# Optimization experiments

Measured on AMD Instinct MI355X. Metric: run time of the kernel, lower is better.

Reference implementation:

```python
import jax, jax.numpy as jnp
import numpy as np

TOPK = 4  # constructor default topk=4


def setup_inputs() -> dict:
    key = jax.random.key(0)
    k_x, k_a, k_b, k_w, k_bias = jax.random.split(key, 5)
    b, s, h, j, a, r = 4, 2048, 2048, 2048, 64, 16
    x = jax.random.normal(k_x, (b, s, h), dtype=jnp.float32)
    A = jax.random.normal(k_a, (a, r, h), dtype=jnp.float32) * 0.02   # adapter down-proj bank
    B = jax.random.normal(k_b, (a, j, r), dtype=jnp.float32) * 0.02   # adapter up-proj bank
    W = jax.random.normal(k_w, (j, h), dtype=jnp.float32) * 0.02      # base Linear weight
    bias = jax.random.normal(k_bias, (j,), dtype=jnp.float32) * 0.02  # base Linear bias
    return {"x": x, "A": A, "B": B, "W": W, "bias": bias}


def reference(x, A, B, W, bias):
    # vecs: per-adapter low-rank projections of each token. [b,s,a,r]
    vecs = jnp.einsum('arh,bsh->bsar', A, x)
    # routing score = L2 norm over rank dim. [b,s,a]
    arrows = jnp.linalg.norm(vecs, axis=-1)
    # top-k adapters per token -> uniform 1/topk routing weights (scatter of a constant,
    # so no gradient flows through the routing weights, matching torch semantics).
    _, idx = jax.lax.top_k(arrows, TOPK)                     # [b,s,topk]
    routes = jax.nn.one_hot(idx, arrows.shape[-1], dtype=x.dtype).sum(-2) / TOPK  # [b,s,a]
    # weighted combine of selected adapter vecs. [b,s,r]
    v = jnp.einsum('bsa,bsar->bsr', routes, vecs)
    # delta = (routes-weighted B) applied to v; contract over a then r without
    # materializing the [b,s,j,r] intermediate. [b,s,j]
    delta = jnp.einsum('bsa,ajr,bsr->bsj', routes, B, v)
    base = jnp.einsum('bsh,jh->bsj', x, W) + bias
    return base + delta
```

## Files before the change

kernel.cpp:

```cpp
#include <hip/hip_runtime.h>
#include <hip/hip_bf16.h>
#include <stdint.h>

#define TOKENS 8192
#define H 2048
#define JDIM 2048
#define NADAPT 64
#define RANK 16
#define KG 1024
#define KTOT 3072
#define NT2 48
#define NT1 64

typedef __bf16 v8bf __attribute__((ext_vector_type(8)));
typedef float v4f __attribute__((ext_vector_type(4)));
typedef unsigned short us8 __attribute__((ext_vector_type(8)));
typedef unsigned short us4 __attribute__((ext_vector_type(4)));

__device__ __forceinline__ unsigned short f2bf(float f) {
  union { __bf16 b; unsigned short u; } c; c.b = (__bf16)f; return c.u;
}
__device__ __forceinline__ float bf2f(unsigned short u) {
  union { unsigned int u; float f; } c; c.u = ((unsigned int)u) << 16; return c.f;
}

__device__ __forceinline__ us8 pack8(float4 a, float4 b) {
  us8 r;
  r[0]=f2bf(a.x); r[1]=f2bf(a.y); r[2]=f2bf(a.z); r[3]=f2bf(a.w);
  r[4]=f2bf(b.x); r[5]=f2bf(b.y); r[6]=f2bf(b.z); r[7]=f2bf(b.w);
  return r;
}

__device__ __forceinline__ void split8(float4 a, float4 b, us8& h, us8& l) {
  float v[8] = {a.x, a.y, a.z, a.w, b.x, b.y, b.z, b.w};
  #pragma unroll
  for (int i = 0; i < 8; ++i) {
    h[i] = f2bf(v[i]);
    l[i] = f2bf(v[i] - bf2f(h[i]));
  }
}

__global__ void cast_x_split_kernel(const float* __restrict__ x,
                                    unsigned short* __restrict__ XG,
                                    unsigned short* __restrict__ XLO) {
  int idx = blockIdx.x * 256 + threadIdx.x;
  int row = idx >> 8;
  int cg  = idx & 255;
  const float4* s = (const float4*)(x + ((size_t)row << 11) + ((size_t)cg << 3));
  float4 a = s[0], b = s[1];
  us8 h, l;
  split8(a, b, h, l);
  *(us8*)(XG  + (size_t)row * KTOT + ((size_t)cg << 3)) = h;
  *(us8*)(XLO + (size_t)row * H    + ((size_t)cg << 3)) = l;
}

__global__ void cast_a_split_kernel(const float* __restrict__ A,
                                    unsigned short* __restrict__ Ahi,
                                    unsigned short* __restrict__ Alo) {
  int idx = blockIdx.x * 256 + threadIdx.x;
  int row = idx >> 8;
  int cg  = idx & 255;
  const float4* s = (const float4*)(A + ((size_t)row << 11) + ((size_t)cg << 3));
  float4 a = s[0], b = s[1];
  us8 h, l;
  split8(a, b, h, l);
  *(us8*)(Ahi + (size_t)row * H + ((size_t)cg << 3)) = h;
  *(us8*)(Alo + (size_t)row * H + ((size_t)cg << 3)) = l;
}

__global__ void cast2048_kernel(const float* __restrict__ src,
                                unsigned short* __restrict__ dst, int dstld) {
  int idx = blockIdx.x * 256 + threadIdx.x;
  int row = idx >> 8;
  int cg  = idx & 255;
  const float4* s = (const float4*)(src + ((size_t)row << 11) + ((size_t)cg << 3));
  float4 a = s[0], b = s[1];
  *(us8*)(dst + (size_t)row * dstld + ((size_t)cg << 3)) = pack8(a, b);
}

__global__ void cast_b_kernel(const float* __restrict__ Bsrc,
                              unsigned short* __restrict__ WB) {
  int idx = blockIdx.x * 256 + threadIdx.x;
  int a = idx >> 11, j = idx & 2047;
  const float4* s = (const float4*)(Bsrc + (((size_t)a << 11) + j) * RANK);
  float4 f0 = s[0], f1 = s[1], f2 = s[2], f3 = s[3];
  us8* d = (us8*)(WB + (size_t)j * KTOT + H + a * RANK);
  d[0] = pack8(f0, f1);
  d[1] = pack8(f2, f3);
}

__global__ void route_kernel(const float* __restrict__ vecs,
                             unsigned short* __restrict__ XG) {
  __shared__ float vsh[4][16];
  int wave = threadIdx.x >> 6, lane = threadIdx.x & 63;
  int t = blockIdx.x * 4 + wave;
  const float* vrow = vecs + (size_t)t * KG;
  const float4* vp = (const float4*)(vrow + lane * RANK);
  float4 q0 = vp[0], q1 = vp[1], q2 = vp[2], q3 = vp[3];
  float ss = q0.x*q0.x + q0.y*q0.y + q0.z*q0.z + q0.w*q0.w
           + q1.x*q1.x + q1.y*q1.y + q1.z*q1.z + q1.w*q1.w
           + q2.x*q2.x + q2.y*q2.y + q2.z*q2.z + q2.w*q2.w
           + q3.x*q3.x + q3.y*q3.y + q3.z*q3.z + q3.w*q3.w;
  float arr = ss;
  int sel[4];
  #pragma unroll
  for (int k = 0; k < 4; ++k) {
    float m = arr; int mi = lane;
    #pragma unroll
    for (int o = 32; o > 0; o >>= 1) {
      float om = __shfl_xor(m, o);
      int oi  = __shfl_xor(mi, o);
      if (om > m || (om == m && oi < mi)) { m = om; mi = oi; }
    }
    sel[k] = mi;
    if (lane == mi) arr = -3.0e38f;
  }
  if (lane < 16) {
    float s = vrow[sel[0]*RANK + lane] + vrow[sel[1]*RANK + lane]
            + vrow[sel[2]*RANK + lane] + vrow[sel[3]*RANK + lane];
    vsh[wave][lane] = 0.0625f * s;
  }
  __syncthreads();
  bool on = (lane == sel[0]) | (lane == sel[1]) | (lane == sel[2]) | (lane == sel[3]);
  us8 lo, hi;
  #pragma unroll
  for (int r = 0; r < 8; ++r) lo[r] = on ? f2bf(vsh[wave][r])     : (unsigned short)0;
  #pragma unroll
  for (int r = 0; r < 8; ++r) hi[r] = on ? f2bf(vsh[wave][r + 8]) : (unsigned short)0;
  us8* d = (us8*)(XG + (size_t)t * KTOT + H + lane * RANK);
  d[0] = lo; d[1] = hi;
}

__device__ __forceinline__ void gload_lds16(const void* gsrc, void* ldst) {
  __builtin_amdgcn_global_load_lds(
      (const __attribute__((address_space(1))) unsigned int*)gsrc,
      (__attribute__((address_space(3))) unsigned int*)ldst, 16, 0, 0);
}

#define BAR() asm volatile("s_waitcnt lgkmcnt(0)\n\ts_barrier" ::: "memory")
#define VM2() asm volatile("s_waitcnt vmcnt(2)" ::: "memory")
#define VM3() asm volatile("s_waitcnt vmcnt(3)" ::: "memory")
#define VM8() asm volatile("s_waitcnt vmcnt(8)" ::: "memory")
#define P1() __builtin_amdgcn_s_setprio(1)
#define P0() __builtin_amdgcn_s_setprio(0)

#define MM1(mi, xf, bv) do {                                                   \
  acc[mi][0] = __builtin_amdgcn_mfma_f32_16x16x32_bf16(xf, bv[0], acc[mi][0], 0, 0, 0); \
  acc[mi][1] = __builtin_amdgcn_mfma_f32_16x16x32_bf16(xf, bv[1], acc[mi][1], 0, 0, 0); \
  acc[mi][2] = __builtin_amdgcn_mfma_f32_16x16x32_bf16(xf, bv[2], acc[mi][2], 0, 0, 0); \
  acc[mi][3] = __builtin_amdgcn_mfma_f32_16x16x32_bf16(xf, bv[3], acc[mi][3], 0, 0, 0); \
} while (0)

#define LD1(off) (*(const v8bf*)(Lb + (off)))

#define S_XH1(b, kel) gload_lds16(XhB + (size_t)srow * KTOT + (kel) + scol, Lb + (b)*49152 + tid*16)
#define S_XH2(b, kel) gload_lds16(XhB + (size_t)(srow + 128) * KTOT + (kel) + scol, Lb + (b)*49152 + 8192 + tid*16)
#define S_XL1(b, kel) gload_lds16(XlB + (size_t)srow * H + (kel) + scol, Lb + (b)*49152 + 16384 + tid*16)
#define S_XL2(b, kel) gload_lds16(XlB + (size_t)(srow + 128) * H + (kel) + scol, Lb + (b)*49152 + 24576 + tid*16)
#define S_AH1(b, kel) gload_lds16(AhB + (size_t)srow * H + (kel) + scol, Lb + (b)*49152 + 32768 + tid*16)
#define S_AL1(b, kel) gload_lds16(AlB + (size_t)srow * H + (kel) + scol, Lb + (b)*49152 + 40960 + tid*16)

#define TILE1(c, n, kn) do {                                                   \
                                                       \
  xh[0] = LD1((c)*49152 + abyte);                                              \
  xh[1] = LD1((c)*49152 + abyte + 1024);                                       \
  xh[2] = LD1((c)*49152 + abyte + 2048);                                       \
  xh[3] = LD1((c)*49152 + abyte + 3072);                                       \
  ah[0] = LD1((c)*49152 + 32768 + bbyte);                                      \
  ah[1] = LD1((c)*49152 + 32768 + bbyte + 1024);                               \
  ah[2] = LD1((c)*49152 + 32768 + bbyte + 2048);                               \
  ah[3] = LD1((c)*49152 + 32768 + bbyte + 3072);                               \
  S_XH1(n, kn); S_XH2(n, kn);                                                  \
  BAR(); P1(); MM1(0, xh[0], ah); MM1(1, xh[1], ah);                           \
               MM1(2, xh[2], ah); MM1(3, xh[3], ah); P0(); VM2(); BAR();       \
                                                       \
  al[0] = LD1((c)*49152 + 40960 + bbyte);                                      \
  al[1] = LD1((c)*49152 + 40960 + bbyte + 1024);                               \
  al[2] = LD1((c)*49152 + 40960 + bbyte + 2048);                               \
  al[3] = LD1((c)*49152 + 40960 + bbyte + 3072);                               \
  S_AH1(n, kn); S_XL1(n, kn);                                                  \
  BAR(); P1(); MM1(0, xh[0], al); MM1(1, xh[1], al);                           \
               MM1(2, xh[2], al); MM1(3, xh[3], al); P0(); BAR();              \
                                                       \
  xl[0] = LD1((c)*49152 + 16384 + abyte);                                      \
  xl[1] = LD1((c)*49152 + 16384 + abyte + 1024);                               \
  xl[2] = LD1((c)*49152 + 16384 + abyte + 2048);                               \
  xl[3] = LD1((c)*49152 + 16384 + abyte + 3072);                               \
  S_XL2(n, kn); S_AL1(n, kn);                                                  \
  BAR(); P1(); MM1(0, xl[0], ah); MM1(1, xl[1], ah);                           \
               MM1(2, xl[2], ah); MM1(3, xl[3], ah); P0(); VM3(); BAR();       \
} while (0)

__global__ __launch_bounds__(512, 1) void gemm1_8ph_kernel(
    const unsigned short* __restrict__ Xhi,
    const unsigned short* __restrict__ Xlo,
    const unsigned short* __restrict__ Ahi,
    const unsigned short* __restrict__ Alo,
    float* __restrict__ C) {
  __shared__ char Ls[98304];
  char* Lb = Ls;
  const int tid = threadIdx.x;
  const int lane = tid & 63, wid = tid >> 6;
  const int wr = wid >> 1, wc = wid & 1;
  const int rA = lane & 15, grp = lane >> 4;
  const int grpx = (grp ^ ((rA >> 1) & 3)) << 4;

  const int bid = blockIdx.x;
  const int g = bid & 7, r = bid >> 3;
  const int bm = g * 4 + (r & 3), bn = r >> 2;

  const unsigned short* XhB = Xhi + (size_t)(bm * 256) * KTOT;
  const unsigned short* XlB = Xlo + (size_t)(bm * 256) * H;
  const unsigned short* AhB = Ahi + (size_t)(bn * 128) * H;
  const unsigned short* AlB = Alo + (size_t)(bn * 128) * H;

  const int srow = tid >> 2;
  const int scol = ((tid & 3) ^ ((tid >> 3) & 3)) << 3;

  const int abyte = (wr * 64 + rA) * 64 + grpx;
  const int bbyte = (wc * 64 + rA) * 64 + grpx;

  v4f acc[4][4];
  #pragma unroll
  for (int i = 0; i < 4; ++i)
    #pragma unroll
    for (int j = 0; j < 4; ++j)
      acc[i][j] = (v4f){0.f, 0.f, 0.f, 0.f};
  v8bf xh[4], xl[4], ah[4], al[4];

  S_XH1(0, 0); S_XH2(0, 0); S_AH1(0, 0); S_XL1(0, 0); S_XL2(0, 0); S_AL1(0, 0);
  VM3(); BAR();

  #pragma unroll 1
  for (int t = 0; t < NT1; t += 2) {
    const int ka = (t + 1) * 32;
    const int kb = (t + 2 < NT1 ? t + 2 : NT1 - 1) * 32;
    TILE1(0, 1, ka);
    TILE1(1, 0, kb);
  }

  const int row0 = bm * 256 + wr * 64 + (grp << 2);
  const int col0 = bn * 128 + wc * 64 + rA;
  #pragma unroll
  for (int mi = 0; mi < 4; ++mi)
    #pragma unroll
    for (int j = 0; j < 4; ++j)
      #pragma unroll
      for (int q = 0; q < 4; ++q)
        C[(size_t)(row0 + mi * 16 + q) * KG + col0 + j * 16] = acc[mi][j][q];
}

#define STAGE(regionUS, panel, kelem) do {                                        \
  gload_lds16((panel) + aoff0 + (kelem), (char*)(regionUS) + tid * 16);           \
  gload_lds16((panel) + aoff1 + (kelem), (char*)(regionUS) + 8192 + tid * 16);    \
} while (0)

#define PHASE(mh, RAr, RBr, ISSUE, DOVM) do {                                     \
  if ((mh) == 0) {                                                                \
    _Pragma("unroll")                                                             \
    for (int j = 0; j < 4; ++j)                                                   \
      bfr[j] = *(const v8bf*)((const char*)(RBr) + bbyte + j * 1024);             \
  }                                                                               \
  _Pragma("unroll")                                                               \
  for (int i = 0; i < 4; ++i)                                                     \
    af[i] = *(const v8bf*)((const char*)(RAr) + abyte + ((mh)*4 + i) * 1024);     \
  ISSUE;                                                                          \
  BAR();                                                                          \
  P1();                                                                           \
  _Pragma("unroll")                                                               \
  for (int i = 0; i < 4; ++i)                                                     \
    _Pragma("unroll")                                                             \
    for (int j = 0; j < 4; ++j)                                                   \
      acc[(mh)*4 + i][j] = __builtin_amdgcn_mfma_f32_16x16x32_bf16(               \
          af[i], bfr[j], acc[(mh)*4 + i][j], 0, 0, 0);                            \
  P0();                                                                           \
  DOVM;                                                                           \
  BAR();                                                                          \
} while (0)

__global__ __launch_bounds__(512, 1) void gemm2_8ph_kernel(
    const unsigned short* __restrict__ Xg, const unsigned short* __restrict__ Wb,
    float* __restrict__ C, const float* __restrict__ bias) {
  __shared__ unsigned short lds[65536];
  const int tid = threadIdx.x;
  const int lane = tid & 63, wid = tid >> 6;
  const int wr = wid >> 2, wc = wid & 3;
  const int rA = lane & 15, grp = lane >> 4;
  const int grpx = (grp ^ ((rA >> 1) & 3)) << 4;

  const int bid = blockIdx.x;
  const int g = bid & 7, r = bid >> 3;
  const int bm = g * 4 + (r & 3), bn = r >> 2;

  const unsigned short* Ap = Xg + (size_t)(bm * 256) * KTOT;
  const unsigned short* Bp = Wb + (size_t)(bn * 256) * KTOT;

  const int srow = tid >> 2;
  const int scol = ((tid & 3) ^ ((tid >> 3) & 3)) << 3;
  const size_t aoff0 = (size_t)srow * KTOT + scol;
  const size_t aoff1 = (size_t)(srow + 128) * KTOT + scol;

  unsigned short* A0k0 = lds;
  unsigned short* A0k1 = lds + 8192;
  unsigned short* B0k0 = lds + 16384;
  unsigned short* B0k1 = lds + 24576;
  unsigned short* A1k0 = lds + 32768;
  unsigned short* A1k1 = lds + 40960;
  unsigned short* B1k0 = lds + 49152;
  unsigned short* B1k1 = lds + 57344;

  const int abyte = (wr * 128 + rA) * 64 + grpx;
  const int bbyte = (wc * 64 + rA) * 64 + grpx;

  v4f acc[8][4];
  #pragma unroll
  for (int i = 0; i < 8; ++i)
    #pragma unroll
    for (int j = 0; j < 4; ++j)
      acc[i][j] = (v4f){0.f, 0.f, 0.f, 0.f};
  v8bf af[4], bfr[4];

  STAGE(A0k0, Ap, 0);
  STAGE(B0k0, Bp, 0);
  STAGE(A0k1, Ap, 32);
  STAGE(B0k1, Bp, 32);
  STAGE(A1k0, Ap, 64);
  STAGE(B1k0, Bp, 64);
  VM8();
  BAR();

  #pragma unroll 1
  for (int t = 0; t < NT2; t += 2) {
    const int k1a = (t + 1) * 64 + 32;
    const int k0a = (t + 2 < NT2 ? t + 2 : NT2 - 1) * 64;
    const int k1b = (t + 2 < NT2 ? t + 2 : NT2 - 1) * 64 + 32;
    const int k0b = (t + 3 < NT2 ? t + 3 : NT2 - 1) * 64;
    PHASE(0, A0k0, B0k0, STAGE(A1k1, Ap, k1a), ((void)0));
    PHASE(1, A0k0, B0k0, STAGE(B1k1, Bp, k1a), VM8());
    PHASE(0, A0k1, B0k1, STAGE(A0k0, Ap, k0a), ((void)0));
    PHASE(1, A0k1, B0k1, STAGE(B0k0, Bp, k0a), VM8());
    PHASE(0, A1k0, B1k0, STAGE(A0k1, Ap, k1b), ((void)0));
    PHASE(1, A1k0, B1k0, STAGE(B0k1, Bp, k1b), VM8());
    PHASE(0, A1k1, B1k1, STAGE(A1k0, Ap, k0b), ((void)0));
    PHASE(1, A1k1, B1k1, STAGE(B1k0, Bp, k0b), VM8());
  }

  const int row0 = bm * 256 + wr * 128 + (grp << 2);
  const int col0 = bn * 256 + wc * 64 + rA;
  float bv[4];
  #pragma unroll
  for (int j = 0; j < 4; ++j) bv[j] = bias[col0 + j * 16];
  #pragma unroll
  for (int mi = 0; mi < 8; ++mi)
    #pragma unroll
    for (int j = 0; j < 4; ++j)
      #pragma unroll
      for (int q = 0; q < 4; ++q)
        C[(size_t)(row0 + mi * 16 + q) * JDIM + col0 + j * 16] = acc[mi][j][q] + bv[j];
}

extern "C" void kernel_launch(void* const* d_in, const int* in_sizes, int n_in,
                              void* d_out, int out_size, void* d_ws, size_t ws_size,
                              hipStream_t stream) {
  const float* x    = (const float*)d_in[0];
  const float* A    = (const float*)d_in[1];
  const float* Bb   = (const float*)d_in[2];
  const float* W    = (const float*)d_in[3];
  const float* bias = (const float*)d_in[4];
  float* out = (float*)d_out;

  char* ws = (char*)d_ws;
  unsigned short* XG  = (unsigned short*)ws;
  unsigned short* WB  = (unsigned short*)(ws + (size_t)48 * 1024 * 1024);
  unsigned short* Ahi = (unsigned short*)(ws + (size_t)60 * 1024 * 1024);
  unsigned short* Alo = (unsigned short*)(ws + (size_t)64 * 1024 * 1024);
  float* vecs         = (float*)d_out;
  unsigned short* XLO = (unsigned short*)((char*)d_out + (size_t)32 * 1024 * 1024);

  cast_x_split_kernel<<<TOKENS, 256, 0, stream>>>(x, XG, XLO);
  cast_a_split_kernel<<<KG, 256, 0, stream>>>(A, Ahi, Alo);
  cast2048_kernel<<<JDIM, 256, 0, stream>>>(W, WB, KTOT);
  cast_b_kernel<<<512, 256, 0, stream>>>(Bb, WB);

  gemm1_8ph_kernel<<<256, 512, 0, stream>>>(XG, XLO, Ahi, Alo, vecs);

  route_kernel<<<TOKENS / 4, 256, 0, stream>>>(vecs, XG);

  gemm2_8ph_kernel<<<256, 512, 0, stream>>>(XG, WB, out, bias);
}
```

Before: 222.0 us.

## Software-pipeline LDS fragment loads ahead of MFMAs in both GEMM kernels

gemm1 moves from a 2-buffer to a 3-buffer LDS ring (147KB) with prefetch distance two, and reorders each phase so MFMAs run first and the next fragments are read from LDS afterwards. gemm2 double-buffers its A fragments in registers and loads the next phase's fragments after the current MFMAs. Both kernels replace the lgkmcnt-waiting barriers with plain barriers and looser vmcnt waits, so more global and LDS traffic stays in flight during MFMA work. The cost is higher LDS and register use, plus a risk of hazards if the relaxed waits do not cover every dependency.

```diff
diff --git a/kernel.cpp b/kernel.cpp
--- a/kernel.cpp
+++ b/kernel.cpp
@@ -137,9 +137,10 @@
       (__attribute__((address_space(3))) unsigned int*)ldst, 16, 0, 0);
 }
 
-#define BAR() asm volatile("s_waitcnt lgkmcnt(0)\n\ts_barrier" ::: "memory")
-#define VM2() asm volatile("s_waitcnt vmcnt(2)" ::: "memory")
-#define VM3() asm volatile("s_waitcnt vmcnt(3)" ::: "memory")
+#define BAR()  asm volatile("s_waitcnt lgkmcnt(0)\n\ts_barrier" ::: "memory")
+#define BARO() asm volatile("s_barrier" ::: "memory")
+#define VM4() asm volatile("s_waitcnt vmcnt(4)" ::: "memory")
+#define VM6() asm volatile("s_waitcnt vmcnt(6)" ::: "memory")
 #define VM8() asm volatile("s_waitcnt vmcnt(8)" ::: "memory")
 #define P1() __builtin_amdgcn_s_setprio(1)
 #define P0() __builtin_amdgcn_s_setprio(0)
@@ -151,45 +152,12 @@
   acc[mi][3] = __builtin_amdgcn_mfma_f32_16x16x32_bf16(xf, bv[3], acc[mi][3], 0, 0, 0); \
 } while (0)
 
-#define LD1(off) (*(const v8bf*)(Lb + (off)))
-
-#define S_XH1(b, kel) gload_lds16(XhB + (size_t)srow * KTOT + (kel) + scol, Lb + (b)*49152 + tid*16)
-#define S_XH2(b, kel) gload_lds16(XhB + (size_t)(srow + 128) * KTOT + (kel) + scol, Lb + (b)*49152 + 8192 + tid*16)
-#define S_XL1(b, kel) gload_lds16(XlB + (size_t)srow * H + (kel) + scol, Lb + (b)*49152 + 16384 + tid*16)
-#define S_XL2(b, kel) gload_lds16(XlB + (size_t)(srow + 128) * H + (kel) + scol, Lb + (b)*49152 + 24576 + tid*16)
-#define S_AH1(b, kel) gload_lds16(AhB + (size_t)srow * H + (kel) + scol, Lb + (b)*49152 + 32768 + tid*16)
-#define S_AL1(b, kel) gload_lds16(AlB + (size_t)srow * H + (kel) + scol, Lb + (b)*49152 + 40960 + tid*16)
-
-#define TILE1(c, n, kn) do {                                                   \
-                                                       \
-  xh[0] = LD1((c)*49152 + abyte);                                              \
-  xh[1] = LD1((c)*49152 + abyte + 1024);                                       \
-  xh[2] = LD1((c)*49152 + abyte + 2048);                                       \
-  xh[3] = LD1((c)*49152 + abyte + 3072);                                       \
-  ah[0] = LD1((c)*49152 + 32768 + bbyte);                                      \
-  ah[1] = LD1((c)*49152 + 32768 + bbyte + 1024);                               \
-  ah[2] = LD1((c)*49152 + 32768 + bbyte + 2048);                               \
-  ah[3] = LD1((c)*49152 + 32768 + bbyte + 3072);                               \
-  S_XH1(n, kn); S_XH2(n, kn);                                                  \
-  BAR(); P1(); MM1(0, xh[0], ah); MM1(1, xh[1], ah);                           \
-               MM1(2, xh[2], ah); MM1(3, xh[3], ah); P0(); VM2(); BAR();       \
-                                                       \
-  al[0] = LD1((c)*49152 + 40960 + bbyte);                                      \
-  al[1] = LD1((c)*49152 + 40960 + bbyte + 1024);                               \
-  al[2] = LD1((c)*49152 + 40960 + bbyte + 2048);                               \
-  al[3] = LD1((c)*49152 + 40960 + bbyte + 3072);                               \
-  S_AH1(n, kn); S_XL1(n, kn);                                                  \
-  BAR(); P1(); MM1(0, xh[0], al); MM1(1, xh[1], al);                           \
-               MM1(2, xh[2], al); MM1(3, xh[3], al); P0(); BAR();              \
-                                                       \
-  xl[0] = LD1((c)*49152 + 16384 + abyte);                                      \
-  xl[1] = LD1((c)*49152 + 16384 + abyte + 1024);                               \
-  xl[2] = LD1((c)*49152 + 16384 + abyte + 2048);                               \
-  xl[3] = LD1((c)*49152 + 16384 + abyte + 3072);                               \
-  S_XL2(n, kn); S_AL1(n, kn);                                                  \
-  BAR(); P1(); MM1(0, xl[0], ah); MM1(1, xl[1], ah);                           \
-               MM1(2, xl[2], ah); MM1(3, xl[3], ah); P0(); VM3(); BAR();       \
-} while (0)
+#define S_XH1(B, kel) gload_lds16(XhB + (size_t)srow * KTOT + (kel) + scol, (B) + tid*16)
+#define S_XH2(B, kel) gload_lds16(XhB + (size_t)(srow + 128) * KTOT + (kel) + scol, (B) + 8192 + tid*16)
+#define S_XL1(B, kel) gload_lds16(XlB + (size_t)srow * H + (kel) + scol, (B) + 16384 + tid*16)
+#define S_XL2(B, kel) gload_lds16(XlB + (size_t)(srow + 128) * H + (kel) + scol, (B) + 24576 + tid*16)
+#define S_AH1(B, kel) gload_lds16(AhB + (size_t)srow * H + (kel) + scol, (B) + 32768 + tid*16)
+#define S_AL1(B, kel) gload_lds16(AlB + (size_t)srow * H + (kel) + scol, (B) + 40960 + tid*16)
 
 __global__ __launch_bounds__(512, 1) void gemm1_8ph_kernel(
     const unsigned short* __restrict__ Xhi,
@@ -197,8 +165,7 @@
     const unsigned short* __restrict__ Ahi,
     const unsigned short* __restrict__ Alo,
     float* __restrict__ C) {
-  __shared__ char Ls[98304];
-  char* Lb = Ls;
+  __shared__ char Ls[147456];
   const int tid = threadIdx.x;
   const int lane = tid & 63, wid = tid >> 6;
   const int wr = wid >> 1, wc = wid & 1;
@@ -220,6 +187,10 @@
   const int abyte = (wr * 64 + rA) * 64 + grpx;
   const int bbyte = (wc * 64 + rA) * 64 + grpx;
 
+  char* bufA = Ls;
+  char* bufB = Ls + 49152;
+  char* bufC = Ls + 98304;
+
   v4f acc[4][4];
   #pragma unroll
   for (int i = 0; i < 4; ++i)
@@ -228,15 +199,35 @@
       acc[i][j] = (v4f){0.f, 0.f, 0.f, 0.f};
   v8bf xh[4], xl[4], ah[4], al[4];
 
-  S_XH1(0, 0); S_XH2(0, 0); S_AH1(0, 0); S_XL1(0, 0); S_XL2(0, 0); S_AL1(0, 0);
-  VM3(); BAR();
+  S_XH1(bufA, 0); S_XH2(bufA, 0); S_AH1(bufA, 0); S_XL1(bufA, 0); S_XL2(bufA, 0); S_AL1(bufA, 0);
+  S_XH1(bufB, 32); S_XH2(bufB, 32); S_AH1(bufB, 32); S_XL1(bufB, 32); S_XL2(bufB, 32); S_AL1(bufB, 32);
+  VM8(); BAR();
+  #pragma unroll
+  for (int i = 0; i < 4; ++i) xh[i] = *(const v8bf*)(bufA + abyte + i * 1024);
+  #pragma unroll
+  for (int j = 0; j < 4; ++j) ah[j] = *(const v8bf*)(bufA + 32768 + bbyte + j * 1024);
 
   #pragma unroll 1
-  for (int t = 0; t < NT1; t += 2) {
-    const int ka = (t + 1) * 32;
-    const int kb = (t + 2 < NT1 ? t + 2 : NT1 - 1) * 32;
-    TILE1(0, 1, ka);
-    TILE1(1, 0, kb);
+  for (int t = 0; t < NT1; ++t) {
+    const int kel = (t + 2 < NT1 ? t + 2 : NT1 - 1) * 32;
+    P1(); MM1(0, xh[0], ah); MM1(1, xh[1], ah); MM1(2, xh[2], ah); MM1(3, xh[3], ah); P0();
+    #pragma unroll
+    for (int j = 0; j < 4; ++j) al[j] = *(const v8bf*)(bufA + 40960 + bbyte + j * 1024);
+    S_XH1(bufC, kel); S_XH2(bufC, kel);
+    VM4(); BARO();
+    P1(); MM1(0, xh[0], al); MM1(1, xh[1], al); MM1(2, xh[2], al); MM1(3, xh[3], al); P0();
+    #pragma unroll
+    for (int i = 0; i < 4; ++i) xl[i] = *(const v8bf*)(bufA + 16384 + abyte + i * 1024);
+    S_AH1(bufC, kel); S_XL1(bufC, kel);
+    VM4(); BARO();
+    P1(); MM1(0, xl[0], ah); MM1(1, xl[1], ah); MM1(2, xl[2], ah); MM1(3, xl[3], ah); P0();
+    #pragma unroll
+    for (int i = 0; i < 4; ++i) xh[i] = *(const v8bf*)(bufB + abyte + i * 1024);
+    #pragma unroll
+    for (int j = 0; j < 4; ++j) ah[j] = *(const v8bf*)(bufB + 32768 + bbyte + j * 1024);
+    S_XL2(bufC, kel); S_AL1(bufC, kel);
+    VM4(); BARO();
+    char* tmp = bufA; bufA = bufB; bufB = bufC; bufC = tmp;
   }
 
   const int row0 = bm * 256 + wr * 64 + (grp << 2);
@@ -255,27 +246,39 @@
   gload_lds16((panel) + aoff1 + (kelem), (char*)(regionUS) + 8192 + tid * 16);    \
 } while (0)
 
-#define PHASE(mh, RAr, RBr, ISSUE, DOVM) do {                                     \
-  if ((mh) == 0) {                                                                \
-    _Pragma("unroll")                                                             \
-    for (int j = 0; j < 4; ++j)                                                   \
-      bfr[j] = *(const v8bf*)((const char*)(RBr) + bbyte + j * 1024);             \
-  }                                                                               \
-  _Pragma("unroll")                                                               \
-  for (int i = 0; i < 4; ++i)                                                     \
-    af[i] = *(const v8bf*)((const char*)(RAr) + abyte + ((mh)*4 + i) * 1024);     \
-  ISSUE;                                                                          \
-  BAR();                                                                          \
+#define PH2A(AFC, RAn, AFN, STG) do {                                             \
   P1();                                                                           \
   _Pragma("unroll")                                                               \
   for (int i = 0; i < 4; ++i)                                                     \
     _Pragma("unroll")                                                             \
     for (int j = 0; j < 4; ++j)                                                   \
-      acc[(mh)*4 + i][j] = __builtin_amdgcn_mfma_f32_16x16x32_bf16(               \
-          af[i], bfr[j], acc[(mh)*4 + i][j], 0, 0, 0);                            \
+      acc[i][j] = __builtin_amdgcn_mfma_f32_16x16x32_bf16(                        \
+          AFC[i], bfr[j], acc[i][j], 0, 0, 0);                                    \
   P0();                                                                           \
-  DOVM;                                                                           \
-  BAR();                                                                          \
+  _Pragma("unroll")                                                               \
+  for (int i = 0; i < 4; ++i)                                                     \
+    AFN[i] = *(const v8bf*)((const char*)(RAn) + abyte + (4 + i) * 1024);         \
+  STG;                                                                            \
+  VM6(); BARO();                                                                  \
+} while (0)
+
+#define PH2B(AFC, RBn, RAn, AFN, STG) do {                                        \
+  P1();                                                                           \
+  _Pragma("unroll")                                                               \
+  for (int i = 0; i < 4; ++i)                                                     \
+    _Pragma("unroll")                                                             \
+    for (int j = 0; j < 4; ++j)                                                   \
+      acc[4 + i][j] = __builtin_amdgcn_mfma_f32_16x16x32_bf16(                    \
+          AFC[i], bfr[j], acc[4 + i][j], 0, 0, 0);                                \
+  P0();                                                                           \
+  _Pragma("unroll")                                                               \
+  for (int j = 0; j < 4; ++j)                                                     \
+    bfr[j] = *(const v8bf*)((const char*)(RBn) + bbyte + j * 1024);               \
+  _Pragma("unroll")                                                               \
+  for (int i = 0; i < 4; ++i)                                                     \
+    AFN[i] = *(const v8bf*)((const char*)(RAn) + abyte + i * 1024);               \
+  STG;                                                                            \
+  VM6(); BARO();                                                                  \
 } while (0)
 
 __global__ __launch_bounds__(512, 1) void gemm2_8ph_kernel(
@@ -318,7 +321,7 @@
     #pragma unroll
     for (int j = 0; j < 4; ++j)
       acc[i][j] = (v4f){0.f, 0.f, 0.f, 0.f};
-  v8bf af[4], bfr[4];
+  v8bf afA[4], afB[4], bfr[4];
 
   STAGE(A0k0, Ap, 0);
   STAGE(B0k0, Bp, 0);
@@ -328,6 +331,10 @@
   STAGE(B1k0, Bp, 64);
   VM8();
   BAR();
+  #pragma unroll
+  for (int i = 0; i < 4; ++i) afA[i] = *(const v8bf*)((const char*)A0k0 + abyte + i * 1024);
+  #pragma unroll
+  for (int j = 0; j < 4; ++j) bfr[j] = *(const v8bf*)((const char*)B0k0 + bbyte + j * 1024);
 
   #pragma unroll 1
   for (int t = 0; t < NT2; t += 2) {
@@ -335,14 +342,14 @@
     const int k0a = (t + 2 < NT2 ? t + 2 : NT2 - 1) * 64;
     const int k1b = (t + 2 < NT2 ? t + 2 : NT2 - 1) * 64 + 32;
     const int k0b = (t + 3 < NT2 ? t + 3 : NT2 - 1) * 64;
-    PHASE(0, A0k0, B0k0, STAGE(A1k1, Ap, k1a), ((void)0));
-    PHASE(1, A0k0, B0k0, STAGE(B1k1, Bp, k1a), VM8());
-    PHASE(0, A0k1, B0k1, STAGE(A0k0, Ap, k0a), ((void)0));
-    PHASE(1, A0k1, B0k1, STAGE(B0k0, Bp, k0a), VM8());
-    PHASE(0, A1k0, B1k0, STAGE(A0k1, Ap, k1b), ((void)0));
-    PHASE(1, A1k0, B1k0, STAGE(B0k1, Bp, k1b), VM8());
-    PHASE(0, A1k1, B1k1, STAGE(A1k0, Ap, k0b), ((void)0));
-    PHASE(1, A1k1, B1k1, STAGE(B1k0, Bp, k0b), VM8());
+    PH2A(afA, A0k0, afB, STAGE(A1k1, Ap, k1a));
+    PH2B(afB, B0k1, A0k1, afA, STAGE(B1k1, Bp, k1a));
+    PH2A(afA, A0k1, afB, STAGE(A0k0, Ap, k0a));
+    PH2B(afB, B1k0, A1k0, afA, STAGE(B0k0, Bp, k0a));
+    PH2A(afA, A1k0, afB, STAGE(A0k1, Ap, k1b));
+    PH2B(afB, B1k1, A1k1, afA, STAGE(B0k1, Bp, k1b));
+    PH2A(afA, A1k1, afB, STAGE(A1k0, Ap, k0b));
+    PH2B(afB, B0k0, A0k0, afA, STAGE(B1k0, Bp, k0b));
   }
 
   const int row0 = bm * 256 + wr * 128 + (grp << 2);
```

After: 213.1 us. -4.0%, faster.
